# Optimization experiments

Measured on AMD Instinct MI355X. Metric: run time of the kernel, lower is better.

The kernel has to match this reference:

```python
import jax, jax.numpy as jnp
import numpy as np


def _log_g(x):
    # log of g(x) = x + 0.5 for x >= 0, sigmoid(x) for x < 0
    return jnp.where(x >= 0, jnp.log(jax.nn.relu(x) + 0.5), -jax.nn.softplus(-x))


def setup_inputs() -> dict:
    key = jax.random.key(0)
    k1, k2 = jax.random.split(key)
    B, S, D = 4, 4096, 1024
    x = jax.random.normal(k1, (B, S, D), dtype=jnp.float32)
    # torch Linear(dim, 2*dim, bias=False) weight layout: [out, in]
    W = jax.random.normal(k2, (2 * D, D), dtype=jnp.float32) * (1.0 / np.sqrt(D))
    return {"x": x, "W": W}


def reference(x, W):
    # x: [B, S, D], W: [2D, D]
    hg = jnp.einsum('bsd,ed->bse', x, W)            # [B, S, 2D]
    hidden, gate = jnp.split(hg, 2, axis=-1)        # each [B, S, D]

    log_coeffs = -jax.nn.softplus(gate)             # log(1 - sigmoid(gate))
    log_z = -jax.nn.softplus(-gate)                 # log(sigmoid(gate))
    log_values = log_z + _log_g(hidden)

    # Heinsen associative scan in log space over the sequence axis
    a_star = jnp.cumsum(log_coeffs, axis=1)
    log_h = a_star + jax.lax.cumlogsumexp(log_values - a_star, axis=1)
    out = jnp.exp(log_h)                            # [B, S, D]; to_out is Identity
    return out
```

## Files before the change

### kernel.cpp

```cpp
#include <hip/hip_runtime.h>
#include <hip/hip_bf16.h>
#include <hip/hip_fp16.h>
#include <cstdint>

typedef unsigned short us;
typedef us   us4 __attribute__((ext_vector_type(4)));
typedef short s8v __attribute__((ext_vector_type(8)));
typedef float f4v __attribute__((ext_vector_type(4)));
typedef __fp16 pk2 __attribute__((ext_vector_type(2)));

#define BB 4
#define SS 4096
#define DD 1024
#define MM (BB * SS)
#define NN (2 * DD)
#define KK DD

#define BM 128
#define BN 128
#define BK 64

#define CHUNK 32
#define NC (SS / CHUNK)
#define BDD (BB * DD)
#define DQ (DD / 4)

__device__ inline us f2bf(float f) {
  unsigned u = __float_as_uint(f);
  u += 0x7fffu + ((u >> 16) & 1u);
  return (us)(u >> 16);
}

__global__ __launch_bounds__(256) void cvt_both(const float* __restrict__ x,
                                                const float* __restrict__ W,
                                                us* __restrict__ xb,
                                                us* __restrict__ wb,
                                                long nx) {
  long i = ((long)blockIdx.x * 256 + threadIdx.x) * 4;
  const float* in;
  us* out;
  if (i < nx) { in = x + i; out = xb + i; }
  else        { in = W + (i - nx); out = wb + (i - nx); }
  float4 a = *(const float4*)in;
  us4 o;
  o[0] = f2bf(a.x); o[1] = f2bf(a.y); o[2] = f2bf(a.z); o[3] = f2bf(a.w);
  *(us4*)out = o;
}

#define GLD16(g, l)                                                        \
  __builtin_amdgcn_global_load_lds(                                        \
      (const __attribute__((address_space(1))) void*)(g),                  \
      (__attribute__((address_space(3))) void*)(l), 16, 0, 0)

__device__ inline void gate_cv(float hid, float gat, float& coef, float& v) {
  float e = __expf(gat);
  coef = __builtin_amdgcn_rcpf(1.0f + e);
  float z = 1.0f - coef;
  float eh = __expf(hid < 0.0f ? hid : 0.0f);
  float gneg = eh * __builtin_amdgcn_rcpf(1.0f + eh);
  float g = (hid >= 0.0f) ? (hid + 0.5f) : gneg;
  v = z * g;
}

__global__ __launch_bounds__(256) void gemm_fused(const us* __restrict__ A,
                                                  const us* __restrict__ B,
                                                  unsigned* __restrict__ cv,
                                                  float* __restrict__ cp,
                                                  float* __restrict__ ch) {
  __shared__ __align__(16) us smem[BM * BK + BN * BK];
  us* As = smem;
  us* Bs = smem + BM * BK;
  unsigned* T = (unsigned*)smem;

  const int tid  = threadIdx.x;
  const int lane = tid & 63;
  const int w    = tid >> 6;
  const int wm   = w & 1;
  const int wn   = w >> 1;
  const long bm  = (long)blockIdx.x * BM;
  const int  d0  = blockIdx.y * 64;

  const int srow = lane >> 3;
  const int sseg = (lane & 7) ^ srow;

  const int fr = lane & 15;
  const int fq = lane >> 4;

  int aoff[4][2], boff[4][2];
#pragma unroll
  for (int mt = 0; mt < 4; ++mt) {
    int row = wm * 64 + mt * 16 + fr;
#pragma unroll
    for (int kk = 0; kk < 2; ++kk) {
      int seg = kk * 4 + fq;
      aoff[mt][kk] = row * BK + ((seg ^ (row & 7)) * 8);
    }
  }
#pragma unroll
  for (int nt = 0; nt < 4; ++nt) {
    int row = wn * 64 + nt * 16 + fr;
#pragma unroll
    for (int kk = 0; kk < 2; ++kk) {
      int seg = kk * 4 + fq;
      boff[nt][kk] = row * BK + ((seg ^ (row & 7)) * 8);
    }
  }

  f4v acc[4][4] = {};

  const us* Ap[4];
  const us* Bp[4];
#pragma unroll
  for (int i = 0; i < 4; ++i) {
    int lr = w * 32 + i * 8 + srow;
    Ap[i] = A + (bm + lr) * (long)KK + sseg * 8;
    int wrow = d0 + ((lr >> 5) << 4) + (lr & 15) + (((lr >> 4) & 1) << 10);
    Bp[i] = B + (long)wrow * KK + sseg * 8;
  }

  for (int kt = 0; kt < KK / BK; ++kt) {
    __syncthreads();
#pragma unroll
    for (int i = 0; i < 4; ++i) {
      GLD16(Ap[i], &As[(w * 32 + i * 8) * BK]);
      GLD16(Bp[i], &Bs[(w * 32 + i * 8) * BK]);
      Ap[i] += BK;
      Bp[i] += BK;
    }
    __syncthreads();

#pragma unroll
    for (int kk = 0; kk < 2; ++kk) {
      s8v af[4], bf[4];
#pragma unroll
      for (int mt = 0; mt < 4; ++mt) af[mt] = *(const s8v*)&As[aoff[mt][kk]];
#pragma unroll
      for (int nt = 0; nt < 4; ++nt) bf[nt] = *(const s8v*)&Bs[boff[nt][kk]];
#pragma unroll
      for (int mt = 0; mt < 4; ++mt)
#pragma unroll
        for (int nt = 0; nt < 4; ++nt)
          acc[mt][nt] = __builtin_amdgcn_mfma_f32_16x16x32_bf16(
              af[mt], bf[nt], acc[mt][nt], 0, 0, 0);
    }
  }

  __syncthreads();
#pragma unroll
  for (int mt = 0; mt < 4; ++mt) {
    int lr0 = wm * 64 + mt * 16 + fq * 4;
#pragma unroll
    for (int p = 0; p < 2; ++p) {
      int ld = (wn * 2 + p) * 16 + fr;
      f4v hv = acc[mt][2 * p];
      f4v gv = acc[mt][2 * p + 1];
#pragma unroll
      for (int r = 0; r < 4; ++r) {
        float coef, v;
        gate_cv(hv[r], gv[r], coef, v);
        pk2 pk = __builtin_amdgcn_cvt_pkrtz(coef, v);
        T[(lr0 + r) * 64 + ld] = __builtin_bit_cast(unsigned, pk);
      }
    }
  }
  __syncthreads();

#pragma unroll
  for (int j = 0; j < 8; ++j) {
    int chunk = j * 256 + tid;
    int row = chunk >> 4;
    int q   = chunk & 15;
    uint4 val = *(const uint4*)&T[row * 64 + q * 4];
    *(uint4*)(cv + (size_t)(bm + row) * DD + d0 + q * 4) = val;
  }

  {
    const int d = tid & 63;
    const int c = tid >> 6;
    float P = 1.0f, h = 0.0f;
#pragma unroll
    for (int i = 0; i < CHUNK; ++i) {
      unsigned u = T[(c * CHUNK + i) * 64 + d];
      __half2 hv = *(__half2*)&u;
      float cf = __half2float(hv.x);
      h = fmaf(cf, h, __half2float(hv.y));
      P *= cf;
    }
    const int b  = (int)(bm / SS);
    const int cg = (int)((bm % SS) / CHUNK) + c;
    const int idx = cg * BDD + b * DD + d0 + d;
    cp[idx] = P;
    ch[idx] = h;
  }
}

__global__ __launch_bounds__(256) void scan_pass2(const float* __restrict__ cp,
                                                  const float* __restrict__ ch,
                                                  float* __restrict__ carry) {
  const int bd = blockIdx.x * 256 + threadIdx.x;
  float h = 0.0f;
  for (int cb = 0; cb < NC; cb += 16) {
    float p[16], v[16];
#pragma unroll
    for (int i = 0; i < 16; ++i) {
      p[i] = cp[(cb + i) * BDD + bd];
      v[i] = ch[(cb + i) * BDD + bd];
    }
#pragma unroll
    for (int i = 0; i < 16; ++i) {
      carry[(cb + i) * BDD + bd] = h;
      h = fmaf(p[i], h, v[i]);
    }
  }
}

__global__ __launch_bounds__(256) void scan_pass3(const uint4* __restrict__ cv,
                                                  const float* __restrict__ carry,
                                                  float4* __restrict__ out) {
  const int q = threadIdx.x;
  const int c = blockIdx.y;
  const int b = blockIdx.z;
  const size_t rbase = ((size_t)b * SS + (size_t)c * CHUNK) * DQ + q;
  const uint4* base = cv + rbase;
  float4* obase = out + rbase;
  float4 h = *(const float4*)&carry[c * BDD + b * DD + 4 * q];
  for (int tb = 0; tb < CHUNK; tb += 8) {
    uint4 u[8];
#pragma unroll
    for (int j = 0; j < 8; ++j) u[j] = base[(size_t)(tb + j) * DQ];
#pragma unroll
    for (int j = 0; j < 8; ++j) {
      __half2 a0 = *(__half2*)&u[j].x;
      __half2 a1 = *(__half2*)&u[j].y;
      __half2 a2 = *(__half2*)&u[j].z;
      __half2 a3 = *(__half2*)&u[j].w;
      h.x = fmaf(__half2float(a0.x), h.x, __half2float(a0.y));
      h.y = fmaf(__half2float(a1.x), h.y, __half2float(a1.y));
      h.z = fmaf(__half2float(a2.x), h.z, __half2float(a2.y));
      h.w = fmaf(__half2float(a3.x), h.w, __half2float(a3.y));
      obase[(size_t)(tb + j) * DQ] = h;
    }
  }
}

extern "C" void kernel_launch(void* const* d_in, const int* in_sizes, int n_in,
                              void* d_out, int out_size, void* d_ws, size_t ws_size,
                              hipStream_t stream) {
  const float* x = (const float*)d_in[0];
  const float* W = (const float*)d_in[1];
  float4* out = (float4*)d_out;

  const long nx = (long)MM * KK;
  const long nw = (long)NN * KK;

  char* ws = (char*)d_ws;
  unsigned* cv = (unsigned*)ws;      ws += (size_t)MM * DD * sizeof(unsigned);
  us* xb = (us*)ws;                  ws += (size_t)nx * sizeof(us);
  us* wb = (us*)ws;                  ws += (size_t)nw * sizeof(us);
  float* cp = (float*)ws;            ws += (size_t)NC * BDD * sizeof(float);
  float* chh = (float*)ws;           ws += (size_t)NC * BDD * sizeof(float);
  float* carry = (float*)ws;         ws += (size_t)NC * BDD * sizeof(float);

  cvt_both<<<(int)((nx + nw) / 4 / 256), 256, 0, stream>>>(x, W, xb, wb, nx);

  gemm_fused<<<dim3(MM / BM, DD / 64), 256, 0, stream>>>(xb, wb, cv, cp, chh);

  scan_pass2<<<dim3(BDD / 256), 256, 0, stream>>>(cp, chh, carry);
  scan_pass3<<<dim3(1, NC, BB), 256, 0, stream>>>((const uint4*)cv, carry, out);
}
```

Baseline: 226.9 us.

## Fuse all four stages into one persistent cooperative kernel with grid syncs

Replaces the four separate launches (convert, GEMM+gate, carry scan, apply scan) with one persistent cooperative kernel that loops over tiles and separates the phases with grid-wide barriers. The goal is to remove inter-kernel launch gaps and tail effects. The final scan phase is also re-partitioned into float2-wide work items over 1024 blocks. The cost is that the GEMM now runs as a persistent grid capped at 1024 blocks with launch bounds requesting 4 blocks per CU, which may change occupancy. Grid syncs and the serial carry phase running on only 4096 threads could also leave much of the grid idle.

```diff
diff --git a/kernel.cpp b/kernel.cpp
--- a/kernel.cpp
+++ b/kernel.cpp
@@ -1,7 +1,10 @@
 #include <hip/hip_runtime.h>
+#include <hip/hip_cooperative_groups.h>
 #include <hip/hip_bf16.h>
 #include <hip/hip_fp16.h>
 #include <cstdint>
+
+namespace cg = cooperative_groups;
 
 typedef unsigned short us;
 typedef us   us4 __attribute__((ext_vector_type(4)));
@@ -19,16 +22,239 @@
 #define BM 128
 #define BN 128
 #define BK 64
+#define NTILES ((MM / BM) * (DD / 64))
 
 #define CHUNK 32
 #define NC (SS / CHUNK)
 #define BDD (BB * DD)
 #define DQ (DD / 4)
+#define NXW ((long)MM * KK + (long)NN * KK)
+#define NXQ (NXW / 4)
 
 __device__ inline us f2bf(float f) {
   unsigned u = __float_as_uint(f);
   u += 0x7fffu + ((u >> 16) & 1u);
   return (us)(u >> 16);
+}
+
+#define GLD16(g, l)                                                        \
+  __builtin_amdgcn_global_load_lds(                                        \
+      (const __attribute__((address_space(1))) void*)(g),                  \
+      (__attribute__((address_space(3))) void*)(l), 16, 0, 0)
+
+__device__ inline void gate_cv(float hid, float gat, float& coef, float& v) {
+  float e = __expf(gat);
+  coef = __builtin_amdgcn_rcpf(1.0f + e);
+  float z = 1.0f - coef;
+  float eh = __expf(hid < 0.0f ? hid : 0.0f);
+  float gneg = eh * __builtin_amdgcn_rcpf(1.0f + eh);
+  float g = (hid >= 0.0f) ? (hid + 0.5f) : gneg;
+  v = z * g;
+}
+
+__global__ __launch_bounds__(256, 4) void mega(const float* __restrict__ x,
+                                               const float* __restrict__ W,
+                                               us* __restrict__ xb,
+                                               us* __restrict__ wb,
+                                               unsigned* __restrict__ cv,
+                                               float* __restrict__ cp,
+                                               float* __restrict__ ch,
+                                               float* __restrict__ carry,
+                                               float2* __restrict__ out) {
+  cg::grid_group grid = cg::this_grid();
+  const int tid  = threadIdx.x;
+  const int nblk = gridDim.x;
+  const long gsize = (long)nblk * 256;
+  const long gtid  = (long)blockIdx.x * 256 + tid;
+  const long nx = (long)MM * KK;
+
+  for (long q = gtid; q < NXQ; q += gsize) {
+    long i = q * 4;
+    const float* in;
+    us* o;
+    if (i < nx) { in = x + i; o = xb + i; }
+    else        { in = W + (i - nx); o = wb + (i - nx); }
+    float4 a = *(const float4*)in;
+    us4 ov;
+    ov[0] = f2bf(a.x); ov[1] = f2bf(a.y); ov[2] = f2bf(a.z); ov[3] = f2bf(a.w);
+    *(us4*)o = ov;
+  }
+  grid.sync();
+
+  {
+    __shared__ __align__(16) us smem[BM * BK + BN * BK];
+    us* As = smem;
+    us* Bs = smem + BM * BK;
+    unsigned* T = (unsigned*)smem;
+
+    const int lane = tid & 63;
+    const int w    = tid >> 6;
+    const int wm   = w & 1;
+    const int wn   = w >> 1;
+
+    const int srow = lane >> 3;
+    const int sseg = (lane & 7) ^ srow;
+    const int fr = lane & 15;
+    const int fq = lane >> 4;
+
+    int aoff[4][2], boff[4][2];
+#pragma unroll
+    for (int mt = 0; mt < 4; ++mt) {
+      int row = wm * 64 + mt * 16 + fr;
+#pragma unroll
+      for (int kk = 0; kk < 2; ++kk) {
+        int seg = kk * 4 + fq;
+        aoff[mt][kk] = row * BK + ((seg ^ (row & 7)) * 8);
+      }
+    }
+#pragma unroll
+    for (int nt = 0; nt < 4; ++nt) {
+      int row = wn * 64 + nt * 16 + fr;
+#pragma unroll
+      for (int kk = 0; kk < 2; ++kk) {
+        int seg = kk * 4 + fq;
+        boff[nt][kk] = row * BK + ((seg ^ (row & 7)) * 8);
+      }
+    }
+
+    for (int t = blockIdx.x; t < NTILES; t += nblk) {
+      const int bx = t & (MM / BM - 1);
+      const int by = t >> 7;
+      const long bm = (long)bx * BM;
+      const int  d0 = by * 64;
+
+      f4v acc[4][4] = {};
+
+      const us* Ap[4];
+      const us* Bp[4];
+#pragma unroll
+      for (int i = 0; i < 4; ++i) {
+        int lr = w * 32 + i * 8 + srow;
+        Ap[i] = xb + (bm + lr) * (long)KK + sseg * 8;
+        int wrow = d0 + ((lr >> 5) << 4) + (lr & 15) + (((lr >> 4) & 1) << 10);
+        Bp[i] = wb + (long)wrow * KK + sseg * 8;
+      }
+
+      for (int kt = 0; kt < KK / BK; ++kt) {
+        __syncthreads();
+#pragma unroll
+        for (int i = 0; i < 4; ++i) {
+          GLD16(Ap[i], &As[(w * 32 + i * 8) * BK]);
+          GLD16(Bp[i], &Bs[(w * 32 + i * 8) * BK]);
+          Ap[i] += BK;
+          Bp[i] += BK;
+        }
+        __syncthreads();
+
+#pragma unroll
+        for (int kk = 0; kk < 2; ++kk) {
+          s8v af[4], bf[4];
+#pragma unroll
+          for (int mt = 0; mt < 4; ++mt) af[mt] = *(const s8v*)&As[aoff[mt][kk]];
+#pragma unroll
+          for (int nt = 0; nt < 4; ++nt) bf[nt] = *(const s8v*)&Bs[boff[nt][kk]];
+#pragma unroll
+          for (int mt = 0; mt < 4; ++mt)
+#pragma unroll
+            for (int nt = 0; nt < 4; ++nt)
+              acc[mt][nt] = __builtin_amdgcn_mfma_f32_16x16x32_bf16(
+                  af[mt], bf[nt], acc[mt][nt], 0, 0, 0);
+        }
+      }
+
+      __syncthreads();
+#pragma unroll
+      for (int mt = 0; mt < 4; ++mt) {
+        int lr0 = wm * 64 + mt * 16 + fq * 4;
+#pragma unroll
+        for (int p = 0; p < 2; ++p) {
+          int ld = (wn * 2 + p) * 16 + fr;
+          f4v hv = acc[mt][2 * p];
+          f4v gv = acc[mt][2 * p + 1];
+#pragma unroll
+          for (int r = 0; r < 4; ++r) {
+            float coef, v;
+            gate_cv(hv[r], gv[r], coef, v);
+            pk2 pk = __builtin_amdgcn_cvt_pkrtz(coef, v);
+            T[(lr0 + r) * 64 + ld] = __builtin_bit_cast(unsigned, pk);
+          }
+        }
+      }
+      __syncthreads();
+
+#pragma unroll
+      for (int j = 0; j < 8; ++j) {
+        int chunk = j * 256 + tid;
+        int row = chunk >> 4;
+        int q   = chunk & 15;
+        uint4 val = *(const uint4*)&T[row * 64 + q * 4];
+        *(uint4*)(cv + (size_t)(bm + row) * DD + d0 + q * 4) = val;
+      }
+
+      {
+        const int d = tid & 63;
+        const int c = tid >> 6;
+        float P = 1.0f, h = 0.0f;
+#pragma unroll
+        for (int i = 0; i < CHUNK; ++i) {
+          unsigned u = T[(c * CHUNK + i) * 64 + d];
+          __half2 hv = *(__half2*)&u;
+          float cf = __half2float(hv.x);
+          h = fmaf(cf, h, __half2float(hv.y));
+          P *= cf;
+        }
+        const int b  = (int)(bm / SS);
+        const int cg2 = (int)((bm % SS) / CHUNK) + c;
+        const int idx = cg2 * BDD + b * DD + d0 + d;
+        cp[idx] = P;
+        ch[idx] = h;
+      }
+    }
+  }
+  grid.sync();
+
+  for (long bd = gtid; bd < BDD; bd += gsize) {
+    float h = 0.0f;
+    for (int cb = 0; cb < NC; cb += 16) {
+      float p[16], v[16];
+#pragma unroll
+      for (int i = 0; i < 16; ++i) {
+        p[i] = cp[(cb + i) * BDD + bd];
+        v[i] = ch[(cb + i) * BDD + bd];
+      }
+#pragma unroll
+      for (int i = 0; i < 16; ++i) {
+        carry[(cb + i) * BDD + bd] = h;
+        h = fmaf(p[i], h, v[i]);
+      }
+    }
+  }
+  grid.sync();
+
+  for (int r = blockIdx.x; r < 1024; r += nblk) {
+    const int b    = r >> 8;
+    const int rem  = r & 255;
+    const int c    = rem >> 1;
+    const int half = rem & 1;
+    const int dp   = half * 256 + tid;
+    const size_t rbase = ((size_t)b * SS + (size_t)c * CHUNK) * (DD / 2) + dp;
+    const uint2* base = (const uint2*)cv + rbase;
+    float2* obase = out + rbase;
+    float2 h = *(const float2*)&carry[c * BDD + b * DD + 2 * dp];
+    for (int tb = 0; tb < CHUNK; tb += 8) {
+      uint2 u[8];
+#pragma unroll
+      for (int j = 0; j < 8; ++j) u[j] = base[(size_t)(tb + j) * (DD / 2)];
+#pragma unroll
+      for (int j = 0; j < 8; ++j) {
+        __half2 a0 = *(__half2*)&u[j].x;
+        __half2 a1 = *(__half2*)&u[j].y;
+        h.x = fmaf(__half2float(a0.x), h.x, __half2float(a0.y));
+        h.y = fmaf(__half2float(a1.x), h.y, __half2float(a1.y));
+        obase[(size_t)(tb + j) * (DD / 2)] = h;
+      }
+    }
+  }
 }
 
 __global__ __launch_bounds__(256) void cvt_both(const float* __restrict__ x,
@@ -47,21 +273,6 @@
   *(us4*)out = o;
 }
 
-#define GLD16(g, l)                                                        \
-  __builtin_amdgcn_global_load_lds(                                        \
-      (const __attribute__((address_space(1))) void*)(g),                  \
-      (__attribute__((address_space(3))) void*)(l), 16, 0, 0)
-
-__device__ inline void gate_cv(float hid, float gat, float& coef, float& v) {
-  float e = __expf(gat);
-  coef = __builtin_amdgcn_rcpf(1.0f + e);
-  float z = 1.0f - coef;
-  float eh = __expf(hid < 0.0f ? hid : 0.0f);
-  float gneg = eh * __builtin_amdgcn_rcpf(1.0f + eh);
-  float g = (hid >= 0.0f) ? (hid + 0.5f) : gneg;
-  v = z * g;
-}
-
 __global__ __launch_bounds__(256) void gemm_fused(const us* __restrict__ A,
                                                   const us* __restrict__ B,
                                                   unsigned* __restrict__ cv,
@@ -82,7 +293,6 @@
 
   const int srow = lane >> 3;
   const int sseg = (lane & 7) ^ srow;
-
   const int fr = lane & 15;
   const int fq = lane >> 4;
 
@@ -187,8 +397,8 @@
       P *= cf;
     }
     const int b  = (int)(bm / SS);
-    const int cg = (int)((bm % SS) / CHUNK) + c;
-    const int idx = cg * BDD + b * DD + d0 + d;
+    const int cg2 = (int)((bm % SS) / CHUNK) + c;
+    const int idx = cg2 * BDD + b * DD + d0 + d;
     cp[idx] = P;
     ch[idx] = h;
   }
@@ -248,7 +458,6 @@
                               hipStream_t stream) {
   const float* x = (const float*)d_in[0];
   const float* W = (const float*)d_in[1];
-  float4* out = (float4*)d_out;
 
   const long nx = (long)MM * KK;
   const long nw = (long)NN * KK;
@@ -261,10 +470,39 @@
   float* chh = (float*)ws;           ws += (size_t)NC * BDD * sizeof(float);
   float* carry = (float*)ws;         ws += (size_t)NC * BDD * sizeof(float);
 
+  static int s_coop = -1;
+  if (s_coop < 0) {
+    s_coop = 0;
+    int dev = 0;
+    hipGetDevice(&dev);
+    hipDeviceProp_t prop{};
+    if (hipGetDeviceProperties(&prop, dev) == hipSuccess && prop.cooperativeLaunch) {
+      int perCU = 0;
+      if (hipOccupancyMaxActiveBlocksPerMultiprocessor(
+              &perCU, (const void*)mega, 256, 0) == hipSuccess && perCU >= 1) {
+        long cap = (long)perCU * prop.multiProcessorCount;
+        s_coop = (int)(cap < 1024 ? cap : 1024);
+      }
+    }
+    if (s_coop < 16) s_coop = 0;
+  }
+
+  if (s_coop > 0) {
+    const float* xl = x; const float* Wl = W;
+    us* xbl = xb; us* wbl = wb;
+    unsigned* cvl = cv;
+    float* cpl = cp; float* chl = chh; float* cal = carry;
+    float2* outl = (float2*)d_out;
+    void* args[] = {&xl, &Wl, &xbl, &wbl, &cvl, &cpl, &chl, &cal, &outl};
+    if (hipLaunchCooperativeKernel((void*)mega, dim3(s_coop), dim3(256),
+                                   args, 0, stream) == hipSuccess)
+      return;
+    s_coop = 0;
+  }
+
   cvt_both<<<(int)((nx + nw) / 4 / 256), 256, 0, stream>>>(x, W, xb, wb, nx);
-
   gemm_fused<<<dim3(MM / BM, DD / 64), 256, 0, stream>>>(xb, wb, cv, cp, chh);
-
   scan_pass2<<<dim3(BDD / 256), 256, 0, stream>>>(cp, chh, carry);
-  scan_pass3<<<dim3(1, NC, BB), 256, 0, stream>>>((const uint4*)cv, carry, out);
-}
+  scan_pass3<<<dim3(1, NC, BB), 256, 0, stream>>>((const uint4*)cv, carry,
+                                                  (float4*)d_out);
+}
```

New measurement: 511.7 us. 2.26x slower.

## Store packed coef/value intermediates in output buffer and rescan in place

Applied to the files above, without the earlier changes.

The packed fp16 coef/value intermediate now lives in the output buffer instead of a separate workspace region. The final scan pass reads those values and overwrites them with float results in place: each thread handles two channels, the grid gains an x dimension, and all 32 timesteps are loaded before any write. This shrinks the workspace footprint and may improve cache locality. Correctness rests on each thread reading its full chunk before writing, and the __restrict__ qualifiers are dropped to allow the aliasing.

```diff
diff --git a/kernel.cpp b/kernel.cpp
--- a/kernel.cpp
+++ b/kernel.cpp
@@ -23,7 +23,7 @@
 #define CHUNK 32
 #define NC (SS / CHUNK)
 #define BDD (BB * DD)
-#define DQ (DD / 4)
+#define DP (DD / 2)
 
 __device__ inline us f2bf(float f) {
   unsigned u = __float_as_uint(f);
@@ -214,32 +214,27 @@
   }
 }
 
-__global__ __launch_bounds__(256) void scan_pass3(const uint4* __restrict__ cv,
+__global__ __launch_bounds__(256) void scan_pass3(const uint2* cv,
                                                   const float* __restrict__ carry,
-                                                  float4* __restrict__ out) {
-  const int q = threadIdx.x;
+                                                  float2* out) {
+  const int dp = blockIdx.x * 256 + threadIdx.x;
   const int c = blockIdx.y;
   const int b = blockIdx.z;
-  const size_t rbase = ((size_t)b * SS + (size_t)c * CHUNK) * DQ + q;
-  const uint4* base = cv + rbase;
-  float4* obase = out + rbase;
-  float4 h = *(const float4*)&carry[c * BDD + b * DD + 4 * q];
-  for (int tb = 0; tb < CHUNK; tb += 8) {
-    uint4 u[8];
-#pragma unroll
-    for (int j = 0; j < 8; ++j) u[j] = base[(size_t)(tb + j) * DQ];
-#pragma unroll
-    for (int j = 0; j < 8; ++j) {
-      __half2 a0 = *(__half2*)&u[j].x;
-      __half2 a1 = *(__half2*)&u[j].y;
-      __half2 a2 = *(__half2*)&u[j].z;
-      __half2 a3 = *(__half2*)&u[j].w;
-      h.x = fmaf(__half2float(a0.x), h.x, __half2float(a0.y));
-      h.y = fmaf(__half2float(a1.x), h.y, __half2float(a1.y));
-      h.z = fmaf(__half2float(a2.x), h.z, __half2float(a2.y));
-      h.w = fmaf(__half2float(a3.x), h.w, __half2float(a3.y));
-      obase[(size_t)(tb + j) * DQ] = h;
-    }
+  const size_t rbase = ((size_t)b * SS + (size_t)c * CHUNK) * DP + dp;
+  const uint2* base = cv + rbase;
+  float2* obase = out + rbase;
+  float2 h = *(const float2*)&carry[c * BDD + b * DD + 2 * dp];
+
+  uint2 u[CHUNK];
+#pragma unroll
+  for (int t = 0; t < CHUNK; ++t) u[t] = base[(size_t)t * DP];
+#pragma unroll
+  for (int t = 0; t < CHUNK; ++t) {
+    __half2 a  = *(__half2*)&u[t].x;
+    __half2 bq = *(__half2*)&u[t].y;
+    h.x = fmaf(__half2float(a.x),  h.x, __half2float(a.y));
+    h.y = fmaf(__half2float(bq.x), h.y, __half2float(bq.y));
+    obase[(size_t)t * DP] = h;
   }
 }
 
@@ -248,13 +243,13 @@
                               hipStream_t stream) {
   const float* x = (const float*)d_in[0];
   const float* W = (const float*)d_in[1];
-  float4* out = (float4*)d_out;
 
   const long nx = (long)MM * KK;
   const long nw = (long)NN * KK;
 
+  unsigned* cv = (unsigned*)d_out;
+
   char* ws = (char*)d_ws;
-  unsigned* cv = (unsigned*)ws;      ws += (size_t)MM * DD * sizeof(unsigned);
   us* xb = (us*)ws;                  ws += (size_t)nx * sizeof(us);
   us* wb = (us*)ws;                  ws += (size_t)nw * sizeof(us);
   float* cp = (float*)ws;            ws += (size_t)NC * BDD * sizeof(float);
@@ -266,5 +261,6 @@
   gemm_fused<<<dim3(MM / BM, DD / 64), 256, 0, stream>>>(xb, wb, cv, cp, chh);
 
   scan_pass2<<<dim3(BDD / 256), 256, 0, stream>>>(cp, chh, carry);
-  scan_pass3<<<dim3(1, NC, BB), 256, 0, stream>>>((const uint4*)cv, carry, out);
-}
+  scan_pass3<<<dim3(DP / 256, NC, BB), 256, 0, stream>>>((const uint2*)cv, carry,
+                                                         (float2*)d_out);
+}
```

Result: no change. 223.5 us, median of 2 (-1.5%).
